# Kernel optimization log

Hardware: AMD Instinct MI355X
Metric: run time of the kernel (lower is better)

Reference implementation:

```python
import jax, jax.numpy as jnp
import numpy as np

ALPHA = 0.2  # LeakyReLU negative slope
NEG_INF = -1e9


def _build_mask(N, seq_len, seg_len):
    # mask: [4, N, N], matches the torch construction exactly
    eyeN = jnp.eye(N, dtype=jnp.float32)
    m0 = eyeN
    m1 = jnp.zeros((N, N), jnp.float32)
    m1 = m1.at[seq_len:seq_len + seg_len, seq_len:seq_len + seg_len].set(
        1.0 - jnp.eye(seg_len, dtype=jnp.float32))
    m2 = jnp.zeros((N, N), jnp.float32)
    m2 = m2.at[:seq_len, seq_len:seq_len + seg_len].set(1.0)
    m2 = m2.at[seq_len:seq_len + seg_len, :seq_len].set(1.0)
    m3 = jnp.zeros((N, N), jnp.float32)
    m3 = m3.at[seq_len + seg_len:, :seq_len].set(1.0)
    m3 = m3.at[:seq_len, seq_len + seg_len:].set(1.0)
    return jnp.stack([m0, m1, m2, m3], axis=0)


def setup_inputs() -> dict:
    key = jax.random.key(0)
    k_in, k_adj, k_W, k_a1, k_a2 = jax.random.split(key, 5)
    B, N, d_in, d_out = 8, 1024, 256, 256
    inp = jax.random.normal(k_in, (B, N, d_in), dtype=jnp.float32)
    adj = jax.random.randint(k_adj, (B, N, N), 0, 2, dtype=jnp.int32)
    # xavier_uniform with gain=1.414
    def xavier(k, shape, gain=1.414):
        fan_out, fan_in = shape[0], shape[-1]
        bound = gain * np.sqrt(6.0 / (fan_in + fan_out))
        return jax.random.uniform(k, shape, jnp.float32, -bound, bound)
    W = xavier(k_W, (d_out, d_in))          # Linear(in, out, bias=False): y = x @ W.T
    a1 = xavier(k_a1, (4, d_out))           # four Linear(out, 1) weights stacked
    a2 = xavier(k_a2, (4, d_out))
    return {"input": inp, "adj": adj, "W": W, "a1": a1, "a2": a2,
            "seq_len": 512, "seg_len": 256, "gaz_len": 256}


def reference(input, adj, W, a1, a2, seq_len, seg_len, gaz_len):
    B, N, _ = input.shape
    h = jnp.einsum('bnd,od->bno', input, W)            # [B, N, out]
    s1 = jnp.einsum('bno,ko->kbn', h, a1)              # [4, B, N]
    s2 = jnp.einsum('bno,ko->kbn', h, a2)              # [4, B, N]
    e = s1[..., :, None] + s2[..., None, :]            # [4, B, N, N]
    e = jnp.where(e > 0, e, ALPHA * e)                 # LeakyReLU
    mask = _build_mask(N, seq_len, seg_len)            # [4, N, N]
    attention = jnp.einsum('kbij,kij->bij', e, mask)   # weighted sum of 4 score maps
    attention = jnp.where(adj == 0, NEG_INF, attention)
    attention = jax.nn.softmax(attention, axis=2)
    # dropout skipped (eval mode / deterministic reference)
    h_prime = jnp.matmul(attention, h)                 # [B, N, out]
    return jax.nn.elu(h_prime)                         # concat=True path
```

## Files before the change

kernel.cpp:

```cpp
#include <hip/hip_runtime.h>
#include <hip/hip_bf16.h>

#define B_ 8
#define N_ 1024
#define D_ 256
#define M_ (B_ * N_)

typedef __attribute__((ext_vector_type(8))) short bf16x8;
typedef __attribute__((ext_vector_type(8))) unsigned short u16x8;
typedef __attribute__((ext_vector_type(4))) float f32x4;

__device__ __forceinline__ unsigned short f2bf(float f) {
    unsigned int u = __float_as_uint(f);
    u += 0x7fffu + ((u >> 16) & 1u);
    return (unsigned short)(u >> 16);
}
__device__ __forceinline__ unsigned int cvtpk(float lo, float hi) {
    unsigned int r;
    asm("v_cvt_pk_bf16_f32 %0, %1, %2" : "=v"(r) : "v"(lo), "v"(hi));
    return r;
}
__device__ __forceinline__ bf16x8 load8_f32_bf(const float* __restrict__ p) {
    const float4* q = (const float4*)p;
    float4 u = q[0], v = q[1];
    union { unsigned int u4[4]; bf16x8 v8; } c;
    c.u4[0] = cvtpk(u.x, u.y); c.u4[1] = cvtpk(u.z, u.w);
    c.u4[2] = cvtpk(v.x, v.y); c.u4[3] = cvtpk(v.z, v.w);
    return c.v8;
}

__global__ __launch_bounds__(512) void k_hgemm(const float* __restrict__ x,
        const float* __restrict__ W,
        const float* __restrict__ a1, const float* __restrict__ a2,
        const int* __restrict__ adj,
        unsigned short* __restrict__ hT,
        float* __restrict__ s1, float* __restrict__ s2,
        unsigned long long* __restrict__ mask) {
    __shared__ unsigned short xs[32 * 256];
    __shared__ unsigned short tls[8][32][40];
    __shared__ float spart[8][32][9];
    const int tid = threadIdx.x;
    const int wslot = tid >> 6, lane = tid & 63;
    const int mt = (blockIdx.x & 7) * 32 + (blockIdx.x >> 3);
    const int m0 = mt * 32, n0 = wslot * 32;
    char* xc = (char*)xs;

    {
        const int row = tid >> 4, colg = (tid & 15) * 16;
        const float4* xp = (const float4*)(x + (m0 + row) * D_ + colg);
        float4 f0 = xp[0], f1 = xp[1], f2 = xp[2], f3 = xp[3];
        union { unsigned int u4[8]; u16x8 v8[2]; } c;
        c.u4[0] = cvtpk(f0.x, f0.y); c.u4[1] = cvtpk(f0.z, f0.w);
        c.u4[2] = cvtpk(f1.x, f1.y); c.u4[3] = cvtpk(f1.z, f1.w);
        c.u4[4] = cvtpk(f2.x, f2.y); c.u4[5] = cvtpk(f2.z, f2.w);
        c.u4[6] = cvtpk(f3.x, f3.y); c.u4[7] = cvtpk(f3.z, f3.w);
        const int base = row * 512 + colg * 2, sw = (row & 7) << 4;
        *(u16x8*)(xc + ((base) ^ sw))      = c.v8[0];
        *(u16x8*)(xc + ((base + 16) ^ sw)) = c.v8[1];
    }
    __syncthreads();

    const int r = lane & 15, kg = lane >> 4;
    const int sw = (r & 7) << 4;
    const int abase0 = r * 512, abase1 = (16 + r) * 512;
    const float* wb0 = W + (n0 + r) * D_ + kg * 8;
    const float* wb1 = wb0 + 16 * D_;
    f32x4 z = {0.f, 0.f, 0.f, 0.f};
    f32x4 acc00 = z, acc01 = z, acc10 = z, acc11 = z;
    bf16x8 nb0 = load8_f32_bf(wb0);
    bf16x8 nb1 = load8_f32_bf(wb1);
    #pragma unroll
    for (int d0 = 0; d0 < D_; d0 += 32) {
        const int kb = (d0 + kg * 8) * 2;
        bf16x8 a0 = *(const bf16x8*)(xc + ((abase0 + kb) ^ sw));
        bf16x8 a1f = *(const bf16x8*)(xc + ((abase1 + kb) ^ sw));
        bf16x8 b0 = nb0, b1 = nb1;
        if (d0 + 32 < D_) {
            nb0 = load8_f32_bf(wb0 + d0 + 32);
            nb1 = load8_f32_bf(wb1 + d0 + 32);
        }
        acc00 = __builtin_amdgcn_mfma_f32_16x16x32_bf16(a0, b0, acc00, 0, 0, 0);
        acc01 = __builtin_amdgcn_mfma_f32_16x16x32_bf16(a0, b1, acc01, 0, 0, 0);
        acc10 = __builtin_amdgcn_mfma_f32_16x16x32_bf16(a1f, b0, acc10, 0, 0, 0);
        acc11 = __builtin_amdgcn_mfma_f32_16x16x32_bf16(a1f, b1, acc11, 0, 0, 0);
    }
    const int col = lane & 15, rb = (lane >> 4) * 4;
    f32x4 accs[2][2] = {{acc00, acc01}, {acc10, acc11}};
    #pragma unroll
    for (int rt = 0; rt < 2; ++rt)
      #pragma unroll
      for (int ct = 0; ct < 2; ++ct)
        #pragma unroll
        for (int q = 0; q < 4; ++q)
            tls[wslot][rt * 16 + rb + q][ct * 16 + col] = f2bf(accs[rt][ct][q]);
    __syncthreads();

    {
        bf16x8 bfr = {0, 0, 0, 0, 0, 0, 0, 0};
        if (r < 8) {
            const float* ap = (r < 4 ? a1 + r * D_ : a2 + (r - 4) * D_) + n0 + kg * 8;
            bfr = load8_f32_bf(ap);
        }
        bf16x8 af0 = *(const bf16x8*)&tls[wslot][r][kg * 8];
        bf16x8 af1 = *(const bf16x8*)&tls[wslot][16 + r][kg * 8];
        f32x4 s0 = __builtin_amdgcn_mfma_f32_16x16x32_bf16(af0, bfr, z, 0, 0, 0);
        f32x4 s1v = __builtin_amdgcn_mfma_f32_16x16x32_bf16(af1, bfr, z, 0, 0, 0);
        if (col < 8) {
            #pragma unroll
            for (int q = 0; q < 4; ++q) {
                spart[wslot][rb + q][col] = s0[q];
                spart[wslot][16 + rb + q][col] = s1v[q];
            }
        }
    }

    const int bb = m0 >> 10, nbase = m0 & 1023;
    const int ol = lane >> 1, nh = lane & 1;
    unsigned short vv[16];
    #pragma unroll
    for (int q2 = 0; q2 < 16; ++q2) vv[q2] = tls[wslot][nh * 16 + q2][ol];
    u16x8 lo, hi;
    #pragma unroll
    for (int q2 = 0; q2 < 8; ++q2) { lo[q2] = vv[q2]; hi[q2] = vv[8 + q2]; }
    unsigned short* dst = hT + ((size_t)(bb * D_ + n0 + ol)) * N_ + nbase + nh * 16;
    *(u16x8*)dst = lo;
    *(u16x8*)(dst + 8) = hi;

    __syncthreads();
    if (tid < 256) {
        const int row = tid >> 3, s = tid & 7;
        float v = 0.f;
        #pragma unroll
        for (int wv = 0; wv < 8; ++wv) v += spart[wv][row][s];
        if (s < 4) s1[s * M_ + m0 + row] = v;
        else       s2[(s - 4) * M_ + m0 + row] = v;
    }

    {
        const int wrow = m0 + wslot * 4;
        #pragma unroll
        for (int rp = 0; rp < 2; ++rp) {
            int a0v[16], a1v[16];
            const int* r0p = adj + (size_t)(wrow + rp * 2) * N_ + lane;
            const int* r1p = r0p + N_;
            #pragma unroll
            for (int seg = 0; seg < 16; ++seg) {
                a0v[seg] = __builtin_nontemporal_load(r0p + seg * 64);
                a1v[seg] = __builtin_nontemporal_load(r1p + seg * 64);
            }
            unsigned long long w0 = 0, w1 = 0;
            #pragma unroll
            for (int seg = 0; seg < 16; ++seg) {
                unsigned long long b0 = __ballot(a0v[seg] != 0);
                unsigned long long b1 = __ballot(a1v[seg] != 0);
                if (lane == seg) { w0 = b0; w1 = b1; }
            }
            if (lane < 16) {
                mask[(size_t)(wrow + rp * 2) * 16 + lane]     = w0;
                mask[(size_t)(wrow + rp * 2 + 1) * 16 + lane] = w1;
            }
        }
    }
}

__global__ __launch_bounds__(512) void k_fused(
        const unsigned long long* __restrict__ mask,
        const float* __restrict__ s1, const float* __restrict__ s2,
        const unsigned short* __restrict__ hT, float* __restrict__ out) {
    __shared__ unsigned short Pe[32 * 1024];
    __shared__ float invl[32];
    const int b  = blockIdx.x & 7;
    const int i0 = (blockIdx.x >> 3) << 5;
    const int tid = threadIdx.x;

    const int w = tid >> 6, lane = tid & 63;
    const int r = lane & 15, kg = lane >> 4;
    const int o0 = w << 5;
    const unsigned short* hTb = hT + (((size_t)b) << 18);
    const unsigned short* pb0 = hTb + (o0 + r) * N_ + kg * 8;
    const unsigned short* pb1 = pb0 + 16 * N_;
    bf16x8 c00 = *(const bf16x8*)pb0;
    bf16x8 c10 = *(const bf16x8*)pb1;
    bf16x8 c01 = *(const bf16x8*)(pb0 + 32);
    bf16x8 c11 = *(const bf16x8*)(pb1 + 32);

    {
        const int ir = tid >> 4, tj = tid & 15;
        const int i = i0 + ir;
        const int gr = b * N_ + i;
        const float s1i0 = s1[0 * M_ + gr], s1i1 = s1[1 * M_ + gr];
        const float s1i2 = s1[2 * M_ + gr], s1i3 = s1[3 * M_ + gr];
        float base; int ko;
        if (i < 512) {
            if (tj < 8)       { base = 0.f;  ko = -1; }
            else if (tj < 12) { base = s1i2; ko = 2 * M_; }
            else              { base = s1i3; ko = 3 * M_; }
        } else if (i < 768) {
            if (tj < 8)       { base = s1i2; ko = 2 * M_; }
            else if (tj < 12) { base = s1i1; ko = 1 * M_; }
            else              { base = 0.f;  ko = -1; }
        } else {
            if (tj < 8)       { base = s1i3; ko = 3 * M_; }
            else              { base = 0.f;  ko = -1; }
        }
        float dval; { float t = s1i0 + s2[b * N_ + i]; dval = fmaxf(t, 0.2f * t); }
        const unsigned long long m = mask[(size_t)gr * 16 + tj];
        const float* s2k = s2 + b * N_ + (ko < 0 ? 0 : ko) + tj * 64;
        float lsum = 0.f;
        #pragma unroll
        for (int qq = 0; qq < 8; ++qq) {
            const int q8 = (qq + tj) & 7;
            const int j0 = tj * 64 + q8 * 8;
            float sv[8];
            if (ko >= 0) {
                float4 v0 = *(const float4*)(s2k + q8 * 8);
                float4 v1 = *(const float4*)(s2k + q8 * 8 + 4);
                sv[0] = v0.x; sv[1] = v0.y; sv[2] = v0.z; sv[3] = v0.w;
                sv[4] = v1.x; sv[5] = v1.y; sv[6] = v1.z; sv[7] = v1.w;
            } else {
                #pragma unroll
                for (int q = 0; q < 8; ++q) sv[q] = 0.f;
            }
            const unsigned int mb = (unsigned int)(m >> (q8 * 8)) & 0xffu;
            float evv[8];
            #pragma unroll
            for (int q = 0; q < 8; ++q) {
                const int j = j0 + q;
                float t = base + sv[q];
                float att = fmaxf(t, 0.2f * t);
                if (j == i) att = dval;
                const float ev = ((mb >> q) & 1u) ? __expf(att) : 0.f;
                lsum += ev;
                evv[q] = ev;
            }
            union { unsigned int u4[4]; u16x8 v8; } c8;
            c8.u4[0] = cvtpk(evv[0], evv[1]); c8.u4[1] = cvtpk(evv[2], evv[3]);
            c8.u4[2] = cvtpk(evv[4], evv[5]); c8.u4[3] = cvtpk(evv[6], evv[7]);
            *(u16x8*)((char*)Pe + ((ir * 2048 + j0 * 2) ^ ((ir & 7) << 4))) = c8.v8;
        }
        lsum += __shfl_xor(lsum, 1, 64);
        lsum += __shfl_xor(lsum, 2, 64);
        lsum += __shfl_xor(lsum, 4, 64);
        lsum += __shfl_xor(lsum, 8, 64);
        if (tj == 0) invl[ir] = 1.f / lsum;
    }
    __syncthreads();

    f32x4 z = {0.f, 0.f, 0.f, 0.f};
    f32x4 acc00 = z, acc01 = z, acc10 = z, acc11 = z;
    const char* Pc = (const char*)Pe;
    const int sw0 = (r & 7) << 4;
    const int base0 = r * 2048, base1 = (16 + r) * 2048;
    #pragma unroll 2
    for (int k0 = 0; k0 < N_; k0 += 64) {
        int kb = (k0 + kg * 8) * 2;
        bf16x8 a0 = *(const bf16x8*)(Pc + ((base0 + kb) ^ sw0));
        bf16x8 a1f = *(const bf16x8*)(Pc + ((base1 + kb) ^ sw0));
        bf16x8 b0 = c00, b1 = c10;
        if (k0 + 64 < N_) {
            c00 = *(const bf16x8*)(pb0 + k0 + 64);
            c10 = *(const bf16x8*)(pb1 + k0 + 64);
        }
        acc00 = __builtin_amdgcn_mfma_f32_16x16x32_bf16(a0, b0, acc00, 0, 0, 0);
        acc01 = __builtin_amdgcn_mfma_f32_16x16x32_bf16(a0, b1, acc01, 0, 0, 0);
        acc10 = __builtin_amdgcn_mfma_f32_16x16x32_bf16(a1f, b0, acc10, 0, 0, 0);
        acc11 = __builtin_amdgcn_mfma_f32_16x16x32_bf16(a1f, b1, acc11, 0, 0, 0);
        kb = (k0 + 32 + kg * 8) * 2;
        a0 = *(const bf16x8*)(Pc + ((base0 + kb) ^ sw0));
        a1f = *(const bf16x8*)(Pc + ((base1 + kb) ^ sw0));
        b0 = c01; b1 = c11;
        if (k0 + 96 < N_) {
            c01 = *(const bf16x8*)(pb0 + k0 + 96);
            c11 = *(const bf16x8*)(pb1 + k0 + 96);
        }
        acc00 = __builtin_amdgcn_mfma_f32_16x16x32_bf16(a0, b0, acc00, 0, 0, 0);
        acc01 = __builtin_amdgcn_mfma_f32_16x16x32_bf16(a0, b1, acc01, 0, 0, 0);
        acc10 = __builtin_amdgcn_mfma_f32_16x16x32_bf16(a1f, b0, acc10, 0, 0, 0);
        acc11 = __builtin_amdgcn_mfma_f32_16x16x32_bf16(a1f, b1, acc11, 0, 0, 0);
    }
    const int col = lane & 15, rb = (lane >> 4) << 2;
    f32x4 accs[2][2] = {{acc00, acc01}, {acc10, acc11}};
    #pragma unroll
    for (int rt = 0; rt < 2; ++rt) {
        #pragma unroll
        for (int q = 0; q < 4; ++q) {
            const int il = rt * 16 + rb + q;
            const float sc = invl[il];
            #pragma unroll
            for (int ct = 0; ct < 2; ++ct) {
                float v = accs[rt][ct][q] * sc;
                v = v > 0.f ? v : (__expf(v) - 1.f);
                __builtin_nontemporal_store(v,
                    &out[((size_t)(b * N_ + i0 + il)) * D_ + o0 + ct * 16 + col]);
            }
        }
    }
}

extern "C" void kernel_launch(void* const* d_in, const int* in_sizes, int n_in,
                              void* d_out, int out_size, void* d_ws, size_t ws_size,
                              hipStream_t stream) {
    const float* x   = (const float*)d_in[0];
    const int*   adj = (const int*)d_in[1];
    const float* W   = (const float*)d_in[2];
    const float* a1  = (const float*)d_in[3];
    const float* a2  = (const float*)d_in[4];
    float* out = (float*)d_out;

    char* ws = (char*)d_ws;
    unsigned short* hT = (unsigned short*)ws;
    float* s1 = (float*)(ws + (4u << 20));
    float* s2 = (float*)(ws + (4u << 20) + (128u << 10));
    unsigned long long* mask = (unsigned long long*)(ws + (4u << 20) + (512u << 10));

    hipLaunchKernelGGL(k_hgemm, dim3(256), dim3(512), 0, stream, x, W, a1, a2, adj, hT, s1, s2, mask);
    hipLaunchKernelGGL(k_fused, dim3(256), dim3(512), 0, stream, mask, s1, s2, hT, out);
}
```

Before: 40.81 us.

## Fuse projection and attention kernels with per-batch grid barrier

Merges the h-projection/score/mask kernel and the fused attention kernel into one cooperative launch. Each block now computes the 32 rows it later consumes. A software barrier over the 32 blocks of each batch, built from global atomic counters and sense flags, replaces the kernel boundary. The aim is to remove the second launch and the full-device drain between the two stages. In exchange it adds atomic spinning, and the larger combined shared-memory footprint may lower occupancy.

Result: slower. 74.55 us (+82.7%).

```diff
diff --git a/kernel.cpp b/kernel.cpp
--- a/kernel.cpp
+++ b/kernel.cpp
@@ -9,6 +9,9 @@
 typedef __attribute__((ext_vector_type(8))) short bf16x8;
 typedef __attribute__((ext_vector_type(8))) unsigned short u16x8;
 typedef __attribute__((ext_vector_type(4))) float f32x4;
+
+__device__ unsigned bar_cnt[8];
+__device__ unsigned bar_sense[8];
 
 __device__ __forceinline__ unsigned short f2bf(float f) {
     unsigned int u = __float_as_uint(f);
@@ -29,149 +32,168 @@
     return c.v8;
 }
 
-__global__ __launch_bounds__(512) void k_hgemm(const float* __restrict__ x,
-        const float* __restrict__ W,
+__global__ __launch_bounds__(512) void k_all(
+        const float* __restrict__ x, const float* __restrict__ W,
         const float* __restrict__ a1, const float* __restrict__ a2,
         const int* __restrict__ adj,
         unsigned short* __restrict__ hT,
         float* __restrict__ s1, float* __restrict__ s2,
-        unsigned long long* __restrict__ mask) {
+        unsigned long long* __restrict__ mask,
+        float* __restrict__ out) {
     __shared__ unsigned short xs[32 * 256];
     __shared__ unsigned short tls[8][32][40];
     __shared__ float spart[8][32][9];
-    const int tid = threadIdx.x;
-    const int wslot = tid >> 6, lane = tid & 63;
-    const int mt = (blockIdx.x & 7) * 32 + (blockIdx.x >> 3);
-    const int m0 = mt * 32, n0 = wslot * 32;
-    char* xc = (char*)xs;
-
-    {
-        const int row = tid >> 4, colg = (tid & 15) * 16;
-        const float4* xp = (const float4*)(x + (m0 + row) * D_ + colg);
-        float4 f0 = xp[0], f1 = xp[1], f2 = xp[2], f3 = xp[3];
-        union { unsigned int u4[8]; u16x8 v8[2]; } c;
-        c.u4[0] = cvtpk(f0.x, f0.y); c.u4[1] = cvtpk(f0.z, f0.w);
-        c.u4[2] = cvtpk(f1.x, f1.y); c.u4[3] = cvtpk(f1.z, f1.w);
-        c.u4[4] = cvtpk(f2.x, f2.y); c.u4[5] = cvtpk(f2.z, f2.w);
-        c.u4[6] = cvtpk(f3.x, f3.y); c.u4[7] = cvtpk(f3.z, f3.w);
-        const int base = row * 512 + colg * 2, sw = (row & 7) << 4;
-        *(u16x8*)(xc + ((base) ^ sw))      = c.v8[0];
-        *(u16x8*)(xc + ((base + 16) ^ sw)) = c.v8[1];
-    }
-    __syncthreads();
-
-    const int r = lane & 15, kg = lane >> 4;
-    const int sw = (r & 7) << 4;
-    const int abase0 = r * 512, abase1 = (16 + r) * 512;
-    const float* wb0 = W + (n0 + r) * D_ + kg * 8;
-    const float* wb1 = wb0 + 16 * D_;
-    f32x4 z = {0.f, 0.f, 0.f, 0.f};
-    f32x4 acc00 = z, acc01 = z, acc10 = z, acc11 = z;
-    bf16x8 nb0 = load8_f32_bf(wb0);
-    bf16x8 nb1 = load8_f32_bf(wb1);
-    #pragma unroll
-    for (int d0 = 0; d0 < D_; d0 += 32) {
-        const int kb = (d0 + kg * 8) * 2;
-        bf16x8 a0 = *(const bf16x8*)(xc + ((abase0 + kb) ^ sw));
-        bf16x8 a1f = *(const bf16x8*)(xc + ((abase1 + kb) ^ sw));
-        bf16x8 b0 = nb0, b1 = nb1;
-        if (d0 + 32 < D_) {
-            nb0 = load8_f32_bf(wb0 + d0 + 32);
-            nb1 = load8_f32_bf(wb1 + d0 + 32);
-        }
-        acc00 = __builtin_amdgcn_mfma_f32_16x16x32_bf16(a0, b0, acc00, 0, 0, 0);
-        acc01 = __builtin_amdgcn_mfma_f32_16x16x32_bf16(a0, b1, acc01, 0, 0, 0);
-        acc10 = __builtin_amdgcn_mfma_f32_16x16x32_bf16(a1f, b0, acc10, 0, 0, 0);
-        acc11 = __builtin_amdgcn_mfma_f32_16x16x32_bf16(a1f, b1, acc11, 0, 0, 0);
-    }
-    const int col = lane & 15, rb = (lane >> 4) * 4;
-    f32x4 accs[2][2] = {{acc00, acc01}, {acc10, acc11}};
-    #pragma unroll
-    for (int rt = 0; rt < 2; ++rt)
-      #pragma unroll
-      for (int ct = 0; ct < 2; ++ct)
-        #pragma unroll
-        for (int q = 0; q < 4; ++q)
-            tls[wslot][rt * 16 + rb + q][ct * 16 + col] = f2bf(accs[rt][ct][q]);
-    __syncthreads();
-
-    {
-        bf16x8 bfr = {0, 0, 0, 0, 0, 0, 0, 0};
-        if (r < 8) {
-            const float* ap = (r < 4 ? a1 + r * D_ : a2 + (r - 4) * D_) + n0 + kg * 8;
-            bfr = load8_f32_bf(ap);
-        }
-        bf16x8 af0 = *(const bf16x8*)&tls[wslot][r][kg * 8];
-        bf16x8 af1 = *(const bf16x8*)&tls[wslot][16 + r][kg * 8];
-        f32x4 s0 = __builtin_amdgcn_mfma_f32_16x16x32_bf16(af0, bfr, z, 0, 0, 0);
-        f32x4 s1v = __builtin_amdgcn_mfma_f32_16x16x32_bf16(af1, bfr, z, 0, 0, 0);
-        if (col < 8) {
-            #pragma unroll
-            for (int q = 0; q < 4; ++q) {
-                spart[wslot][rb + q][col] = s0[q];
-                spart[wslot][16 + rb + q][col] = s1v[q];
-            }
-        }
-    }
-
-    const int bb = m0 >> 10, nbase = m0 & 1023;
-    const int ol = lane >> 1, nh = lane & 1;
-    unsigned short vv[16];
-    #pragma unroll
-    for (int q2 = 0; q2 < 16; ++q2) vv[q2] = tls[wslot][nh * 16 + q2][ol];
-    u16x8 lo, hi;
-    #pragma unroll
-    for (int q2 = 0; q2 < 8; ++q2) { lo[q2] = vv[q2]; hi[q2] = vv[8 + q2]; }
-    unsigned short* dst = hT + ((size_t)(bb * D_ + n0 + ol)) * N_ + nbase + nh * 16;
-    *(u16x8*)dst = lo;
-    *(u16x8*)(dst + 8) = hi;
-
-    __syncthreads();
-    if (tid < 256) {
-        const int row = tid >> 3, s = tid & 7;
-        float v = 0.f;
-        #pragma unroll
-        for (int wv = 0; wv < 8; ++wv) v += spart[wv][row][s];
-        if (s < 4) s1[s * M_ + m0 + row] = v;
-        else       s2[(s - 4) * M_ + m0 + row] = v;
-    }
-
-    {
-        const int wrow = m0 + wslot * 4;
-        #pragma unroll
-        for (int rp = 0; rp < 2; ++rp) {
-            int a0v[16], a1v[16];
-            const int* r0p = adj + (size_t)(wrow + rp * 2) * N_ + lane;
-            const int* r1p = r0p + N_;
-            #pragma unroll
-            for (int seg = 0; seg < 16; ++seg) {
-                a0v[seg] = __builtin_nontemporal_load(r0p + seg * 64);
-                a1v[seg] = __builtin_nontemporal_load(r1p + seg * 64);
-            }
-            unsigned long long w0 = 0, w1 = 0;
-            #pragma unroll
-            for (int seg = 0; seg < 16; ++seg) {
-                unsigned long long b0 = __ballot(a0v[seg] != 0);
-                unsigned long long b1 = __ballot(a1v[seg] != 0);
-                if (lane == seg) { w0 = b0; w1 = b1; }
-            }
-            if (lane < 16) {
-                mask[(size_t)(wrow + rp * 2) * 16 + lane]     = w0;
-                mask[(size_t)(wrow + rp * 2 + 1) * 16 + lane] = w1;
-            }
-        }
-    }
-}
-
-__global__ __launch_bounds__(512) void k_fused(
-        const unsigned long long* __restrict__ mask,
-        const float* __restrict__ s1, const float* __restrict__ s2,
-        const unsigned short* __restrict__ hT, float* __restrict__ out) {
     __shared__ unsigned short Pe[32 * 1024];
     __shared__ float invl[32];
-    const int b  = blockIdx.x & 7;
-    const int i0 = (blockIdx.x >> 3) << 5;
+
     const int tid = threadIdx.x;
+    const int bid = blockIdx.x;
+    const int b  = bid & 7;
+    const int i0 = (bid >> 3) << 5;
+    const int m0 = b * N_ + i0;
+
+    {
+        const int wslot = tid >> 6, lane = tid & 63;
+        const int n0 = wslot * 32;
+        char* xc = (char*)xs;
+
+        {
+            const int row = tid >> 4, colg = (tid & 15) * 16;
+            const float4* xp = (const float4*)(x + (m0 + row) * D_ + colg);
+            float4 f0 = xp[0], f1 = xp[1], f2 = xp[2], f3 = xp[3];
+            union { unsigned int u4[8]; u16x8 v8[2]; } c;
+            c.u4[0] = cvtpk(f0.x, f0.y); c.u4[1] = cvtpk(f0.z, f0.w);
+            c.u4[2] = cvtpk(f1.x, f1.y); c.u4[3] = cvtpk(f1.z, f1.w);
+            c.u4[4] = cvtpk(f2.x, f2.y); c.u4[5] = cvtpk(f2.z, f2.w);
+            c.u4[6] = cvtpk(f3.x, f3.y); c.u4[7] = cvtpk(f3.z, f3.w);
+            const int base = row * 512 + colg * 2, sw = (row & 7) << 4;
+            *(u16x8*)(xc + ((base) ^ sw))      = c.v8[0];
+            *(u16x8*)(xc + ((base + 16) ^ sw)) = c.v8[1];
+        }
+        __syncthreads();
+
+        const int r = lane & 15, kg = lane >> 4;
+        const int sw = (r & 7) << 4;
+        const int abase0 = r * 512, abase1 = (16 + r) * 512;
+        const float* wb0 = W + (n0 + r) * D_ + kg * 8;
+        const float* wb1 = wb0 + 16 * D_;
+        f32x4 z = {0.f, 0.f, 0.f, 0.f};
+        f32x4 acc00 = z, acc01 = z, acc10 = z, acc11 = z;
+        bf16x8 nb0 = load8_f32_bf(wb0);
+        bf16x8 nb1 = load8_f32_bf(wb1);
+        #pragma unroll
+        for (int d0 = 0; d0 < D_; d0 += 32) {
+            const int kb = (d0 + kg * 8) * 2;
+            bf16x8 a0 = *(const bf16x8*)(xc + ((abase0 + kb) ^ sw));
+            bf16x8 a1f = *(const bf16x8*)(xc + ((abase1 + kb) ^ sw));
+            bf16x8 b0 = nb0, b1 = nb1;
+            if (d0 + 32 < D_) {
+                nb0 = load8_f32_bf(wb0 + d0 + 32);
+                nb1 = load8_f32_bf(wb1 + d0 + 32);
+            }
+            acc00 = __builtin_amdgcn_mfma_f32_16x16x32_bf16(a0, b0, acc00, 0, 0, 0);
+            acc01 = __builtin_amdgcn_mfma_f32_16x16x32_bf16(a0, b1, acc01, 0, 0, 0);
+            acc10 = __builtin_amdgcn_mfma_f32_16x16x32_bf16(a1f, b0, acc10, 0, 0, 0);
+            acc11 = __builtin_amdgcn_mfma_f32_16x16x32_bf16(a1f, b1, acc11, 0, 0, 0);
+        }
+        const int col = lane & 15, rb = (lane >> 4) * 4;
+        f32x4 accs[2][2] = {{acc00, acc01}, {acc10, acc11}};
+        #pragma unroll
+        for (int rt = 0; rt < 2; ++rt)
+          #pragma unroll
+          for (int ct = 0; ct < 2; ++ct)
+            #pragma unroll
+            for (int q = 0; q < 4; ++q)
+                tls[wslot][rt * 16 + rb + q][ct * 16 + col] = f2bf(accs[rt][ct][q]);
+        __syncthreads();
+
+        {
+            bf16x8 bfr = {0, 0, 0, 0, 0, 0, 0, 0};
+            if (r < 8) {
+                const float* ap = (r < 4 ? a1 + r * D_ : a2 + (r - 4) * D_) + n0 + kg * 8;
+                bfr = load8_f32_bf(ap);
+            }
+            bf16x8 af0 = *(const bf16x8*)&tls[wslot][r][kg * 8];
+            bf16x8 af1 = *(const bf16x8*)&tls[wslot][16 + r][kg * 8];
+            f32x4 s0 = __builtin_amdgcn_mfma_f32_16x16x32_bf16(af0, bfr, z, 0, 0, 0);
+            f32x4 s1v = __builtin_amdgcn_mfma_f32_16x16x32_bf16(af1, bfr, z, 0, 0, 0);
+            if (col < 8) {
+                #pragma unroll
+                for (int q = 0; q < 4; ++q) {
+                    spart[wslot][rb + q][col] = s0[q];
+                    spart[wslot][16 + rb + q][col] = s1v[q];
+                }
+            }
+        }
+
+        {
+            const int bb = m0 >> 10, nbase = m0 & 1023;
+            const int ol = lane >> 1, nh = lane & 1;
+            unsigned short vv[16];
+            #pragma unroll
+            for (int q2 = 0; q2 < 16; ++q2) vv[q2] = tls[wslot][nh * 16 + q2][ol];
+            u16x8 lo, hi;
+            #pragma unroll
+            for (int q2 = 0; q2 < 8; ++q2) { lo[q2] = vv[q2]; hi[q2] = vv[8 + q2]; }
+            unsigned short* dst = hT + ((size_t)(bb * D_ + n0 + ol)) * N_ + nbase + nh * 16;
+            *(u16x8*)dst = lo;
+            *(u16x8*)(dst + 8) = hi;
+        }
+
+        __syncthreads();
+        if (tid < 256) {
+            const int row = tid >> 3, s = tid & 7;
+            float v = 0.f;
+            #pragma unroll
+            for (int wv = 0; wv < 8; ++wv) v += spart[wv][row][s];
+            if (s < 4) s1[s * M_ + m0 + row] = v;
+            else       s2[(s - 4) * M_ + m0 + row] = v;
+        }
+
+        {
+            const int wrow = m0 + wslot * 4;
+            #pragma unroll
+            for (int rp = 0; rp < 2; ++rp) {
+                int a0v[16], a1v[16];
+                const int* r0p = adj + (size_t)(wrow + rp * 2) * N_ + lane;
+                const int* r1p = r0p + N_;
+                #pragma unroll
+                for (int seg = 0; seg < 16; ++seg) {
+                    a0v[seg] = __builtin_nontemporal_load(r0p + seg * 64);
+                    a1v[seg] = __builtin_nontemporal_load(r1p + seg * 64);
+                }
+                unsigned long long w0 = 0, w1 = 0;
+                #pragma unroll
+                for (int seg = 0; seg < 16; ++seg) {
+                    unsigned long long b0 = __ballot(a0v[seg] != 0);
+                    unsigned long long b1 = __ballot(a1v[seg] != 0);
+                    if (lane == seg) { w0 = b0; w1 = b1; }
+                }
+                if (lane < 16) {
+                    mask[(size_t)(wrow + rp * 2) * 16 + lane]     = w0;
+                    mask[(size_t)(wrow + rp * 2 + 1) * 16 + lane] = w1;
+                }
+            }
+        }
+    }
+
+    asm volatile("s_waitcnt vmcnt(0)" ::: "memory");
+    __syncthreads();
+    if (tid == 0) {
+        __threadfence();
+        unsigned my = atomicAdd(&bar_sense[b], 0u);
+        unsigned old = atomicAdd(&bar_cnt[b], 1u);
+        if (old == 31u) {
+            atomicExch(&bar_cnt[b], 0u);
+            __threadfence();
+            atomicAdd(&bar_sense[b], 1u);
+        } else {
+            while (atomicAdd(&bar_sense[b], 0u) == my) __builtin_amdgcn_s_sleep(2);
+        }
+        __threadfence();
+    }
+    __syncthreads();
+    asm volatile("" ::: "memory");
 
     const int w = tid >> 6, lane = tid & 63;
     const int r = lane & 15, kg = lane >> 4;
@@ -313,6 +335,7 @@
     float* s2 = (float*)(ws + (4u << 20) + (128u << 10));
     unsigned long long* mask = (unsigned long long*)(ws + (4u << 20) + (512u << 10));
 
-    hipLaunchKernelGGL(k_hgemm, dim3(256), dim3(512), 0, stream, x, W, a1, a2, adj, hT, s1, s2, mask);
-    hipLaunchKernelGGL(k_fused, dim3(256), dim3(512), 0, stream, mask, s1, s2, hT, out);
-}
+    void* args[] = {(void*)&x, (void*)&W, (void*)&a1, (void*)&a2, (void*)&adj,
+                    (void*)&hT, (void*)&s1, (void*)&s2, (void*)&mask, (void*)&out};
+    hipLaunchCooperativeKernel((const void*)k_all, dim3(256), dim3(512), args, 0, stream);
+}
```

## Halve row tile to 16 and double grid size in both kernels

Applied to the files above, without the earlier changes.

Both kernels now process 16 rows per block instead of 32, and each launches 512 blocks instead of 256, so all CUs on the device get work and more wavefronts run concurrently. The fused kernel restructures the softmax phase to use 32 threads per row and rewrites the PV loop with a 4-deep register prefetch of hT fragments. In exchange, every block re-reads the full hT panel for its batch, which doubles global/L2 traffic for B, and each wave issues fewer MFMAs per loaded B fragment.

Result: slower. 60.01 us (+47.0%).

```diff
diff --git a/kernel.cpp b/kernel.cpp
--- a/kernel.cpp
+++ b/kernel.cpp
@@ -36,44 +36,41 @@
         unsigned short* __restrict__ hT,
         float* __restrict__ s1, float* __restrict__ s2,
         unsigned long long* __restrict__ mask) {
-    __shared__ unsigned short xs[32 * 256];
-    __shared__ unsigned short tls[8][32][40];
-    __shared__ float spart[8][32][9];
+    __shared__ unsigned short xs[16 * 256];
+    __shared__ unsigned short tls[8][16][40];
+    __shared__ float spart[8][16][9];
     const int tid = threadIdx.x;
     const int wslot = tid >> 6, lane = tid & 63;
-    const int mt = (blockIdx.x & 7) * 32 + (blockIdx.x >> 3);
-    const int m0 = mt * 32, n0 = wslot * 32;
+    const int b = blockIdx.x & 7;
+    const int m0 = b * N_ + ((blockIdx.x >> 3) << 4);
+    const int n0 = wslot * 32;
     char* xc = (char*)xs;
 
     {
-        const int row = tid >> 4, colg = (tid & 15) * 16;
-        const float4* xp = (const float4*)(x + (m0 + row) * D_ + colg);
-        float4 f0 = xp[0], f1 = xp[1], f2 = xp[2], f3 = xp[3];
-        union { unsigned int u4[8]; u16x8 v8[2]; } c;
+        const int row = tid >> 5, col8 = (tid & 31) * 8;
+        const float4* xp = (const float4*)(x + (m0 + row) * D_ + col8);
+        float4 f0 = xp[0], f1 = xp[1];
+        union { unsigned int u4[4]; u16x8 v8; } c;
         c.u4[0] = cvtpk(f0.x, f0.y); c.u4[1] = cvtpk(f0.z, f0.w);
         c.u4[2] = cvtpk(f1.x, f1.y); c.u4[3] = cvtpk(f1.z, f1.w);
-        c.u4[4] = cvtpk(f2.x, f2.y); c.u4[5] = cvtpk(f2.z, f2.w);
-        c.u4[6] = cvtpk(f3.x, f3.y); c.u4[7] = cvtpk(f3.z, f3.w);
-        const int base = row * 512 + colg * 2, sw = (row & 7) << 4;
-        *(u16x8*)(xc + ((base) ^ sw))      = c.v8[0];
-        *(u16x8*)(xc + ((base + 16) ^ sw)) = c.v8[1];
+        const int base = row * 512 + col8 * 2, sw = (row & 7) << 4;
+        *(u16x8*)(xc + (base ^ sw)) = c.v8;
     }
     __syncthreads();
 
     const int r = lane & 15, kg = lane >> 4;
     const int sw = (r & 7) << 4;
-    const int abase0 = r * 512, abase1 = (16 + r) * 512;
+    const int abase0 = r * 512;
     const float* wb0 = W + (n0 + r) * D_ + kg * 8;
     const float* wb1 = wb0 + 16 * D_;
     f32x4 z = {0.f, 0.f, 0.f, 0.f};
-    f32x4 acc00 = z, acc01 = z, acc10 = z, acc11 = z;
+    f32x4 acc00 = z, acc01 = z;
     bf16x8 nb0 = load8_f32_bf(wb0);
     bf16x8 nb1 = load8_f32_bf(wb1);
     #pragma unroll
     for (int d0 = 0; d0 < D_; d0 += 32) {
         const int kb = (d0 + kg * 8) * 2;
         bf16x8 a0 = *(const bf16x8*)(xc + ((abase0 + kb) ^ sw));
-        bf16x8 a1f = *(const bf16x8*)(xc + ((abase1 + kb) ^ sw));
         bf16x8 b0 = nb0, b1 = nb1;
         if (d0 + 32 < D_) {
             nb0 = load8_f32_bf(wb0 + d0 + 32);
@@ -81,18 +78,16 @@
         }
         acc00 = __builtin_amdgcn_mfma_f32_16x16x32_bf16(a0, b0, acc00, 0, 0, 0);
         acc01 = __builtin_amdgcn_mfma_f32_16x16x32_bf16(a0, b1, acc01, 0, 0, 0);
-        acc10 = __builtin_amdgcn_mfma_f32_16x16x32_bf16(a1f, b0, acc10, 0, 0, 0);
-        acc11 = __builtin_amdgcn_mfma_f32_16x16x32_bf16(a1f, b1, acc11, 0, 0, 0);
     }
     const int col = lane & 15, rb = (lane >> 4) * 4;
-    f32x4 accs[2][2] = {{acc00, acc01}, {acc10, acc11}};
-    #pragma unroll
-    for (int rt = 0; rt < 2; ++rt)
-      #pragma unroll
-      for (int ct = 0; ct < 2; ++ct)
-        #pragma unroll
-        for (int q = 0; q < 4; ++q)
-            tls[wslot][rt * 16 + rb + q][ct * 16 + col] = f2bf(accs[rt][ct][q]);
+    {
+        f32x4 accs2[2] = {acc00, acc01};
+        #pragma unroll
+        for (int ct = 0; ct < 2; ++ct)
+            #pragma unroll
+            for (int q = 0; q < 4; ++q)
+                tls[wslot][rb + q][ct * 16 + col] = f2bf(accs2[ct][q]);
+    }
     __syncthreads();
 
     {
@@ -102,32 +97,28 @@
             bfr = load8_f32_bf(ap);
         }
         bf16x8 af0 = *(const bf16x8*)&tls[wslot][r][kg * 8];
-        bf16x8 af1 = *(const bf16x8*)&tls[wslot][16 + r][kg * 8];
         f32x4 s0 = __builtin_amdgcn_mfma_f32_16x16x32_bf16(af0, bfr, z, 0, 0, 0);
-        f32x4 s1v = __builtin_amdgcn_mfma_f32_16x16x32_bf16(af1, bfr, z, 0, 0, 0);
         if (col < 8) {
             #pragma unroll
-            for (int q = 0; q < 4; ++q) {
-                spart[wslot][rb + q][col] = s0[q];
-                spart[wslot][16 + rb + q][col] = s1v[q];
-            }
-        }
-    }
-
-    const int bb = m0 >> 10, nbase = m0 & 1023;
-    const int ol = lane >> 1, nh = lane & 1;
-    unsigned short vv[16];
-    #pragma unroll
-    for (int q2 = 0; q2 < 16; ++q2) vv[q2] = tls[wslot][nh * 16 + q2][ol];
-    u16x8 lo, hi;
-    #pragma unroll
-    for (int q2 = 0; q2 < 8; ++q2) { lo[q2] = vv[q2]; hi[q2] = vv[8 + q2]; }
-    unsigned short* dst = hT + ((size_t)(bb * D_ + n0 + ol)) * N_ + nbase + nh * 16;
-    *(u16x8*)dst = lo;
-    *(u16x8*)(dst + 8) = hi;
-
-    __syncthreads();
-    if (tid < 256) {
+            for (int q = 0; q < 4; ++q) spart[wslot][rb + q][col] = s0[q];
+        }
+    }
+
+    {
+        const int bb = m0 >> 10, nbase = m0 & 1023;
+        const int ol = lane >> 1, nh = lane & 1;
+        unsigned short vv[8];
+        #pragma unroll
+        for (int q2 = 0; q2 < 8; ++q2) vv[q2] = tls[wslot][nh * 8 + q2][ol];
+        u16x8 v8;
+        #pragma unroll
+        for (int q2 = 0; q2 < 8; ++q2) v8[q2] = vv[q2];
+        unsigned short* dst = hT + ((size_t)(bb * D_ + n0 + ol)) * N_ + nbase + nh * 8;
+        *(u16x8*)dst = v8;
+    }
+
+    __syncthreads();
+    if (tid < 128) {
         const int row = tid >> 3, s = tid & 7;
         float v = 0.f;
         #pragma unroll
@@ -137,28 +128,25 @@
     }
 
     {
-        const int wrow = m0 + wslot * 4;
-        #pragma unroll
-        for (int rp = 0; rp < 2; ++rp) {
-            int a0v[16], a1v[16];
-            const int* r0p = adj + (size_t)(wrow + rp * 2) * N_ + lane;
-            const int* r1p = r0p + N_;
-            #pragma unroll
-            for (int seg = 0; seg < 16; ++seg) {
-                a0v[seg] = __builtin_nontemporal_load(r0p + seg * 64);
-                a1v[seg] = __builtin_nontemporal_load(r1p + seg * 64);
-            }
-            unsigned long long w0 = 0, w1 = 0;
-            #pragma unroll
-            for (int seg = 0; seg < 16; ++seg) {
-                unsigned long long b0 = __ballot(a0v[seg] != 0);
-                unsigned long long b1 = __ballot(a1v[seg] != 0);
-                if (lane == seg) { w0 = b0; w1 = b1; }
-            }
-            if (lane < 16) {
-                mask[(size_t)(wrow + rp * 2) * 16 + lane]     = w0;
-                mask[(size_t)(wrow + rp * 2 + 1) * 16 + lane] = w1;
-            }
+        const int wrow = m0 + wslot * 2;
+        int a0v[16], a1v[16];
+        const int* r0p = adj + (size_t)wrow * N_ + lane;
+        const int* r1p = r0p + N_;
+        #pragma unroll
+        for (int seg = 0; seg < 16; ++seg) {
+            a0v[seg] = __builtin_nontemporal_load(r0p + seg * 64);
+            a1v[seg] = __builtin_nontemporal_load(r1p + seg * 64);
+        }
+        unsigned long long w0 = 0, w1 = 0;
+        #pragma unroll
+        for (int seg = 0; seg < 16; ++seg) {
+            unsigned long long b0 = __ballot(a0v[seg] != 0);
+            unsigned long long b1 = __ballot(a1v[seg] != 0);
+            if (lane == seg) { w0 = b0; w1 = b1; }
+        }
+        if (lane < 16) {
+            mask[(size_t)wrow * 16 + lane]       = w0;
+            mask[(size_t)(wrow + 1) * 16 + lane] = w1;
         }
     }
 }
@@ -167,10 +155,10 @@
         const unsigned long long* __restrict__ mask,
         const float* __restrict__ s1, const float* __restrict__ s2,
         const unsigned short* __restrict__ hT, float* __restrict__ out) {
-    __shared__ unsigned short Pe[32 * 1024];
-    __shared__ float invl[32];
+    __shared__ unsigned short Pe[16 * 1024];
+    __shared__ float invl[16];
     const int b  = blockIdx.x & 7;
-    const int i0 = (blockIdx.x >> 3) << 5;
+    const int i0 = (blockIdx.x >> 3) << 4;
     const int tid = threadIdx.x;
 
     const int w = tid >> 6, lane = tid & 63;
@@ -179,38 +167,41 @@
     const unsigned short* hTb = hT + (((size_t)b) << 18);
     const unsigned short* pb0 = hTb + (o0 + r) * N_ + kg * 8;
     const unsigned short* pb1 = pb0 + 16 * N_;
-    bf16x8 c00 = *(const bf16x8*)pb0;
-    bf16x8 c10 = *(const bf16x8*)pb1;
-    bf16x8 c01 = *(const bf16x8*)(pb0 + 32);
-    bf16x8 c11 = *(const bf16x8*)(pb1 + 32);
-
-    {
-        const int ir = tid >> 4, tj = tid & 15;
+    bf16x8 cB0[4], cB1[4];
+    #pragma unroll
+    for (int j = 0; j < 4; ++j) {
+        cB0[j] = *(const bf16x8*)(pb0 + j * 32);
+        cB1[j] = *(const bf16x8*)(pb1 + j * 32);
+    }
+
+    {
+        const int ir = tid >> 5, tj = tid & 31;
         const int i = i0 + ir;
         const int gr = b * N_ + i;
         const float s1i0 = s1[0 * M_ + gr], s1i1 = s1[1 * M_ + gr];
         const float s1i2 = s1[2 * M_ + gr], s1i3 = s1[3 * M_ + gr];
         float base; int ko;
         if (i < 512) {
-            if (tj < 8)       { base = 0.f;  ko = -1; }
-            else if (tj < 12) { base = s1i2; ko = 2 * M_; }
+            if (tj < 16)      { base = 0.f;  ko = -1; }
+            else if (tj < 24) { base = s1i2; ko = 2 * M_; }
             else              { base = s1i3; ko = 3 * M_; }
         } else if (i < 768) {
-            if (tj < 8)       { base = s1i2; ko = 2 * M_; }
-            else if (tj < 12) { base = s1i1; ko = 1 * M_; }
+            if (tj < 16)      { base = s1i2; ko = 2 * M_; }
+            else if (tj < 24) { base = s1i1; ko = 1 * M_; }
             else              { base = 0.f;  ko = -1; }
         } else {
-            if (tj < 8)       { base = s1i3; ko = 3 * M_; }
+            if (tj < 16)      { base = s1i3; ko = 3 * M_; }
             else              { base = 0.f;  ko = -1; }
         }
         float dval; { float t = s1i0 + s2[b * N_ + i]; dval = fmaxf(t, 0.2f * t); }
-        const unsigned long long m = mask[(size_t)gr * 16 + tj];
-        const float* s2k = s2 + b * N_ + (ko < 0 ? 0 : ko) + tj * 64;
+        const unsigned long long m64 = mask[(size_t)gr * 16 + (tj >> 1)];
+        const unsigned int m32 = (unsigned int)(m64 >> ((tj & 1) * 32));
+        const float* s2k = s2 + b * N_ + (ko < 0 ? 0 : ko) + tj * 32;
         float lsum = 0.f;
         #pragma unroll
-        for (int qq = 0; qq < 8; ++qq) {
-            const int q8 = (qq + tj) & 7;
-            const int j0 = tj * 64 + q8 * 8;
+        for (int qq = 0; qq < 4; ++qq) {
+            const int q8 = (qq + (tj >> 1)) & 3;
+            const int j0 = tj * 32 + q8 * 8;
             float sv[8];
             if (ko >= 0) {
                 float4 v0 = *(const float4*)(s2k + q8 * 8);
@@ -221,7 +212,7 @@
                 #pragma unroll
                 for (int q = 0; q < 8; ++q) sv[q] = 0.f;
             }
-            const unsigned int mb = (unsigned int)(m >> (q8 * 8)) & 0xffu;
+            const unsigned int mb = (m32 >> (q8 * 8)) & 0xffu;
             float evv[8];
             #pragma unroll
             for (int q = 0; q < 8; ++q) {
@@ -242,53 +233,43 @@
         lsum += __shfl_xor(lsum, 2, 64);
         lsum += __shfl_xor(lsum, 4, 64);
         lsum += __shfl_xor(lsum, 8, 64);
+        lsum += __shfl_xor(lsum, 16, 64);
         if (tj == 0) invl[ir] = 1.f / lsum;
     }
     __syncthreads();
 
     f32x4 z = {0.f, 0.f, 0.f, 0.f};
-    f32x4 acc00 = z, acc01 = z, acc10 = z, acc11 = z;
+    f32x4 acc00 = z, acc01 = z;
     const char* Pc = (const char*)Pe;
     const int sw0 = (r & 7) << 4;
-    const int base0 = r * 2048, base1 = (16 + r) * 2048;
-    #pragma unroll 2
-    for (int k0 = 0; k0 < N_; k0 += 64) {
-        int kb = (k0 + kg * 8) * 2;
-        bf16x8 a0 = *(const bf16x8*)(Pc + ((base0 + kb) ^ sw0));
-        bf16x8 a1f = *(const bf16x8*)(Pc + ((base1 + kb) ^ sw0));
-        bf16x8 b0 = c00, b1 = c10;
-        if (k0 + 64 < N_) {
-            c00 = *(const bf16x8*)(pb0 + k0 + 64);
-            c10 = *(const bf16x8*)(pb1 + k0 + 64);
-        }
-        acc00 = __builtin_amdgcn_mfma_f32_16x16x32_bf16(a0, b0, acc00, 0, 0, 0);
-        acc01 = __builtin_amdgcn_mfma_f32_16x16x32_bf16(a0, b1, acc01, 0, 0, 0);
-        acc10 = __builtin_amdgcn_mfma_f32_16x16x32_bf16(a1f, b0, acc10, 0, 0, 0);
-        acc11 = __builtin_amdgcn_mfma_f32_16x16x32_bf16(a1f, b1, acc11, 0, 0, 0);
-        kb = (k0 + 32 + kg * 8) * 2;
-        a0 = *(const bf16x8*)(Pc + ((base0 + kb) ^ sw0));
-        a1f = *(const bf16x8*)(Pc + ((base1 + kb) ^ sw0));
-        b0 = c01; b1 = c11;
-        if (k0 + 96 < N_) {
-            c01 = *(const bf16x8*)(pb0 + k0 + 96);
-            c11 = *(const bf16x8*)(pb1 + k0 + 96);
-        }
-        acc00 = __builtin_amdgcn_mfma_f32_16x16x32_bf16(a0, b0, acc00, 0, 0, 0);
-        acc01 = __builtin_amdgcn_mfma_f32_16x16x32_bf16(a0, b1, acc01, 0, 0, 0);
-        acc10 = __builtin_amdgcn_mfma_f32_16x16x32_bf16(a1f, b0, acc10, 0, 0, 0);
-        acc11 = __builtin_amdgcn_mfma_f32_16x16x32_bf16(a1f, b1, acc11, 0, 0, 0);
+    const int base0 = r * 2048;
+    bf16x8 aN = *(const bf16x8*)(Pc + ((base0 + kg * 16) ^ sw0));
+    for (int k0 = 0; k0 < N_; k0 += 128) {
+        #pragma unroll
+        for (int j = 0; j < 4; ++j) {
+            const int kk = k0 + j * 32;
+            bf16x8 a0 = aN;
+            if (kk + 32 < N_)
+                aN = *(const bf16x8*)(Pc + ((base0 + (kk + 32 + kg * 8) * 2) ^ sw0));
+            bf16x8 b0 = cB0[j], b1 = cB1[j];
+            if (kk + 128 < N_) {
+                cB0[j] = *(const bf16x8*)(pb0 + kk + 128);
+                cB1[j] = *(const bf16x8*)(pb1 + kk + 128);
+            }
+            acc00 = __builtin_amdgcn_mfma_f32_16x16x32_bf16(a0, b0, acc00, 0, 0, 0);
+            acc01 = __builtin_amdgcn_mfma_f32_16x16x32_bf16(a0, b1, acc01, 0, 0, 0);
+        }
     }
     const int col = lane & 15, rb = (lane >> 4) << 2;
-    f32x4 accs[2][2] = {{acc00, acc01}, {acc10, acc11}};
-    #pragma unroll
-    for (int rt = 0; rt < 2; ++rt) {
+    {
+        f32x4 accs2[2] = {acc00, acc01};
         #pragma unroll
         for (int q = 0; q < 4; ++q) {
-            const int il = rt * 16 + rb + q;
+            const int il = rb + q;
             const float sc = invl[il];
             #pragma unroll
             for (int ct = 0; ct < 2; ++ct) {
-                float v = accs[rt][ct][q] * sc;
+                float v = accs2[ct][q] * sc;
                 v = v > 0.f ? v : (__expf(v) - 1.f);
                 __builtin_nontemporal_store(v,
                     &out[((size_t)(b * N_ + i0 + il)) * D_ + o0 + ct * 16 + col]);
@@ -313,6 +294,6 @@
     float* s2 = (float*)(ws + (4u << 20) + (128u << 10));
     unsigned long long* mask = (unsigned long long*)(ws + (4u << 20) + (512u << 10));
 
-    hipLaunchKernelGGL(k_hgemm, dim3(256), dim3(512), 0, stream, x, W, a1, a2, adj, hT, s1, s2, mask);
-    hipLaunchKernelGGL(k_fused, dim3(256), dim3(512), 0, stream, mask, s1, s2, hT, out);
-}
+    hipLaunchKernelGGL(k_hgemm, dim3(512), dim3(512), 0, stream, x, W, a1, a2, adj, hT, s1, s2, mask);
+    hipLaunchKernelGGL(k_fused, dim3(512), dim3(512), 0, stream, mask, s1, s2, hT, out);
+}
```
